# Kernel tuning notes

Hardware: AMD Instinct MI355X
Metric: run time of the kernel (lower is better)

## Reference

```python
import jax, jax.numpy as jnp
import numpy as np

B, S, H, T, E, V, D = 32, 128, 1024, 32, 512, 32000, 256


def setup_inputs() -> dict:
    key = jax.random.key(0)
    ks = jax.random.split(key, 12)
    rn = lambda k, shp, s: jax.random.normal(k, shp, dtype=jnp.float32) * s
    return {
        "fusion_vector": rn(ks[0], (B, S, H), 1.0),
        "hidden_vector": rn(ks[1], (B, H), 1.0),
        "ground_truth_answer_input": rn(ks[2], (B, T, E), 1.0),
        "ground_truth_seq_helper": T,
        "U_w": rn(ks[3], (D, H), 0.02), "U_b": jnp.zeros((D,), jnp.float32),
        "V_w": rn(ks[4], (D, H), 0.02), "V_b": jnp.zeros((D,), jnp.float32),
        "P_w": rn(ks[5], (1, D), 0.02), "P_b": jnp.zeros((1,), jnp.float32),
        "W_ih": rn(ks[6], (3 * H, E + H), 0.02), "b_ih": jnp.zeros((3 * H,), jnp.float32),
        "W_hh": rn(ks[7], (3 * H, H), 0.02), "b_hh": jnp.zeros((3 * H,), jnp.float32),
        "dense_w": rn(ks[8], (V, H), 0.02), "dense_b": jnp.zeros((V,), jnp.float32),
    }


def reference(fusion_vector, hidden_vector, ground_truth_answer_input,
              U_w, U_b, V_w, V_b, P_w, P_b,
              W_ih, b_ih, W_hh, b_hh, dense_w, dense_b,
              ground_truth_seq_helper):
    f = fusion_vector                                  # (B, S, H)
    # V(f) is loop-invariant: precompute tanh(V f) once.
    vf = jnp.tanh(jnp.einsum('bsh,dh->bsd', f, V_w) + V_b)  # (B, S, D)

    def step(h, x):
        # Bilinear attention pooling: q = h (decoder hidden state)
        uh = jnp.tanh(h @ U_w.T + U_b)                 # (B, D)
        scores = jnp.einsum('bsd,d->bs', uh[:, None, :] * vf, P_w[0]) + P_b[0]
        attn = jax.nn.softmax(scores, axis=-1)         # (B, S)
        mix = jnp.einsum('bs,bsh->bh', attn, f)        # (B, H)
        inp = jnp.concatenate([x, mix], axis=1)        # (B, E+H)
        # torch GRUCell: gate order r, z, n
        gx = inp @ W_ih.T + b_ih
        gh = h @ W_hh.T + b_hh
        xr, xz, xn = jnp.split(gx, 3, axis=1)
        hr, hz, hn = jnp.split(gh, 3, axis=1)
        r = jax.nn.sigmoid(xr + hr)
        z = jax.nn.sigmoid(xz + hz)
        n = jnp.tanh(xn + r * hn)
        h_new = (1.0 - z) * n + z * h
        logits = h_new @ dense_w.T + dense_b           # (B, V)
        return h_new, logits

    xs = jnp.swapaxes(ground_truth_answer_input[:, :-1, :], 0, 1)  # (T-1, B, E)
    _, logits = jax.lax.scan(step, hidden_vector, xs)              # (T-1, B, V)
    return jnp.swapaxes(logits, 0, 1)                              # (B, T-1, V)
```

## Files before the change

kernel.cpp:

```cpp
#include <hip/hip_runtime.h>
#include <hip/hip_bf16.h>
#include <math.h>

typedef unsigned short u16;
typedef unsigned long long u64;
typedef __attribute__((ext_vector_type(8))) short short8;
typedef __attribute__((ext_vector_type(4))) float f32x4;
typedef __attribute__((ext_vector_type(2))) _Float16 half2v;

static __device__ __forceinline__ u16 f2b(float x) {
  __hip_bfloat16 h = __float2bfloat16(x);
  return *reinterpret_cast<u16*>(&h);
}
static __device__ __forceinline__ float b2f(u16 u) {
  unsigned int v = ((unsigned int)u) << 16;
  float f;
  __builtin_memcpy(&f, &v, 4);
  return f;
}
static __device__ __forceinline__ u16 f2h(float x) {
  _Float16 h = (_Float16)x;
  u16 u;
  __builtin_memcpy(&u, &h, 2);
  return u;
}
static __device__ __forceinline__ float dot2(unsigned w, unsigned h, float acc) {
  half2v a, b;
  __builtin_memcpy(&a, &w, 4);
  __builtin_memcpy(&b, &h, 4);
#if __has_builtin(__builtin_amdgcn_fdot2)
  return __builtin_amdgcn_fdot2(a, b, acc, false);
#else
  return acc + (float)a[0] * (float)b[0] + (float)a[1] * (float)b[1];
#endif
}

static __device__ __forceinline__ float aldf(const float* p) {
  return __hip_atomic_load(const_cast<float*>(p), __ATOMIC_RELAXED, __HIP_MEMORY_SCOPE_AGENT);
}
static __device__ __forceinline__ void astf(float* p, float v) {
  __hip_atomic_store(p, v, __ATOMIC_RELAXED, __HIP_MEMORY_SCOPE_AGENT);
}
static __device__ __forceinline__ u64 ald8(const u64* p) {
  return __hip_atomic_load(const_cast<u64*>(p), __ATOMIC_RELAXED, __HIP_MEMORY_SCOPE_AGENT);
}
static __device__ __forceinline__ void ast32(unsigned* p, unsigned v) {
  __hip_atomic_store(p, v, __ATOMIC_RELAXED, __HIP_MEMORY_SCOPE_AGENT);
}


__global__ void cvt_flat(const float* __restrict__ s, u16* __restrict__ d, long n) {
  long i = ((long)blockIdx.x * 256 + threadIdx.x) * 4;
  long stride = (long)gridDim.x * 1024;
  for (; i < n; i += stride) {
    float4 v = *(const float4*)(s + i);
    ushort4 o;
    o.x = f2b(v.x); o.y = f2b(v.y); o.z = f2b(v.z); o.w = f2b(v.w);
    *(ushort4*)(d + i) = o;
  }
}

__global__ void cvt_packh(const float* __restrict__ s, unsigned* __restrict__ d, long npairs) {
  long i = (long)blockIdx.x * 256 + threadIdx.x;
  long step = (long)gridDim.x * 256;
  for (; i < npairs; i += step) {
    float2 v = *(const float2*)(s + 2 * i);
    d[i] = (unsigned)f2h(v.x) | ((unsigned)f2h(v.y) << 16);
  }
}

__global__ void cvt_strided(const float* __restrict__ s, u16* __restrict__ d,
                            long total, int lshift, long sstride, long soff) {
  long i = (long)blockIdx.x * 256 + threadIdx.x;
  long step = (long)gridDim.x * 256;
  long mask = (1L << lshift) - 1;
  for (; i < total; i += step) {
    long r = i >> lshift;
    long c = i & mask;
    d[i] = f2b(s[r * sstride + soff + c]);
  }
}

__global__ void cvt_x(const float* __restrict__ gt, u16* __restrict__ d) {
  long idx = (long)blockIdx.x * 256 + threadIdx.x;
  if (idx >= 1024L * 512) return;
  long m = idx >> 9;
  int k = (int)(idx & 511);
  if (m < 992) {
    int tt = (int)(m >> 5), b = (int)(m & 31);
    d[idx] = f2b(gt[((long)b * 32 + tt) * 512 + k]);
  } else {
    d[idx] = 0;
  }
}

template<int EPI>
__global__ __launch_bounds__(256)
void gemm_bt(const u16* __restrict__ A, const u16* __restrict__ B,
             void* __restrict__ C0,
             const float* __restrict__ bias, const float* __restrict__ pw,
             int M, int N, int K) {
  __shared__ u16 As[4096];
  __shared__ u16 Bs[4096];
  const int tid = threadIdx.x;
  const int lane = tid & 63, wid = tid >> 6;

  int gx = gridDim.x, gy = gridDim.y;
  int orig = blockIdx.y * gx + blockIdx.x;
  int G = gx < 8 ? gx : 8;
  int ng = gx / G;
  int full = ng * G * gy;
  int ct, rt;
  if (orig < full) {
    int grp = orig / (G * gy), rem = orig % (G * gy);
    ct = grp * G + rem % G;
    rt = rem / G;
  } else {
    int Gt = gx - ng * G;
    int rem = orig - full;
    ct = ng * G + rem % Gt;
    rt = rem / Gt;
  }
  const long row0 = (long)rt * 128;
  const long col0 = (long)ct * 128;

  const int wm = (wid >> 1) * 64, wn = (wid & 1) * 64;
  const int fr = lane & 15, fq = lane >> 4;
  const int sr = wid * 16 + (lane >> 2);
  const int sc = (lane & 3) * 8;

  const u16* Ag0 = A + (row0 + sr) * (long)K + sc;
  const u16* Ag1 = Ag0 + 64 * (long)K;
  const u16* Bg0 = B + (col0 + sr) * (long)K + sc;
  const u16* Bg1 = Bg0 + 64 * (long)K;

  u16* AsW0 = &As[wid * 512];
  u16* AsW1 = &As[2048 + wid * 512];
  u16* BsW0 = &Bs[wid * 512];
  u16* BsW1 = &Bs[2048 + wid * 512];

  f32x4 acc[4][4];
#pragma unroll
  for (int i = 0; i < 4; ++i)
#pragma unroll
    for (int j = 0; j < 4; ++j) acc[i][j] = {0.f, 0.f, 0.f, 0.f};

  for (int k0 = 0; k0 < K; k0 += 32) {
    __builtin_amdgcn_global_load_lds((const __attribute__((address_space(1))) void*)(Ag0 + k0),
                                     (__attribute__((address_space(3))) void*)AsW0, 16, 0, 0);
    __builtin_amdgcn_global_load_lds((const __attribute__((address_space(1))) void*)(Ag1 + k0),
                                     (__attribute__((address_space(3))) void*)AsW1, 16, 0, 0);
    __builtin_amdgcn_global_load_lds((const __attribute__((address_space(1))) void*)(Bg0 + k0),
                                     (__attribute__((address_space(3))) void*)BsW0, 16, 0, 0);
    __builtin_amdgcn_global_load_lds((const __attribute__((address_space(1))) void*)(Bg1 + k0),
                                     (__attribute__((address_space(3))) void*)BsW1, 16, 0, 0);
    __syncthreads();
    short8 af[4], bfv[4];
#pragma unroll
    for (int i = 0; i < 4; ++i) af[i] = *(const short8*)&As[(wm + i * 16 + fr) * 32 + fq * 8];
#pragma unroll
    for (int i = 0; i < 4; ++i) bfv[i] = *(const short8*)&Bs[(wn + i * 16 + fr) * 32 + fq * 8];
#pragma unroll
    for (int i = 0; i < 4; ++i)
#pragma unroll
      for (int j = 0; j < 4; ++j)
        acc[i][j] = __builtin_amdgcn_mfma_f32_16x16x32_bf16(af[i], bfv[j], acc[i][j], 0, 0, 0);
    __syncthreads();
  }

#pragma unroll
  for (int i = 0; i < 4; ++i)
#pragma unroll
    for (int j = 0; j < 4; ++j)
#pragma unroll
      for (int q = 0; q < 4; ++q) {
        long gr = row0 + wm + i * 16 + fq * 4 + q;
        long gc = col0 + wn + j * 16 + fr;
        float v = acc[i][j][q];
        if constexpr (EPI == 0) {
          ((u16*)C0)[gr * (long)N + gc] = f2b(v);
        } else if constexpr (EPI == 1) {
          ((u16*)C0)[gr * (long)N + gc] = f2b(tanhf(v + bias[gc]) * pw[gc]);
        } else if constexpr (EPI == 2) {
          if (gr < M) ((float*)C0)[gr * (long)N + gc] = v + bias[gc];
        } else {
          if (gr < M) {
            long bb = gr & 31, tt = gr >> 5;
            float o = v + bias[gc];
            __builtin_nontemporal_store(o, &((float*)C0)[(bb * 31 + tt) * (long)N + gc]);
          }
        }
      }
}

__global__ __launch_bounds__(1024)
void persist(const unsigned* __restrict__ WcatH, const float* __restrict__ bcat,
             const u16* __restrict__ wvfb, const u16* __restrict__ FWb,
             const float* __restrict__ GX, const float* __restrict__ pbv,
             const float* __restrict__ h0,
             unsigned* __restrict__ hG32, float* __restrict__ gates,
             u16* __restrict__ Hbuf, unsigned* __restrict__ cnt) {
  const int tid = threadIdx.x;
  const int blk = blockIdx.x;
  const int rg = blk >> 2, bg = blk & 3;
  const int b = blk >> 3, jc = blk & 7;

  __shared__ unsigned wlds[52 * 516];
  __shared__ float hl2[128];
  __shared__ __align__(16) char smem[45056];
  unsigned* hlds = (unsigned*)smem;
  float*    plds = (float*)(smem + 16512 * 4 / 4 + 0);
  plds = (float*)(smem + 16512);
  float* uhl   = (float*)smem;
  float* part  = uhl + 256;
  float* attnv = part + 1024;
  float* gmp   = attnv + 128;

  const float pb0 = pbv[0];
  if (tid < 128) hl2[tid] = h0[b * 1024 + jc * 128 + tid];

  for (int it = tid; it < 52 * 512; it += 1024) {
    int row = it >> 9, idx = it & 511;
    wlds[row * 516 + idx] = WcatH[(long)(rg * 52 + row) * 512 + idx];
  }

  auto xbar = [&](unsigned target) {
    __syncthreads();
    if (tid == 0) {
      __hip_atomic_fetch_add(cnt, 1u, __ATOMIC_RELAXED, __HIP_MEMORY_SCOPE_AGENT);
      while (__hip_atomic_load(cnt, __ATOMIC_RELAXED, __HIP_MEMORY_SCOPE_AGENT) < target) {
        __builtin_amdgcn_s_sleep(2);
      }
    }
    __syncthreads();
  };
  xbar(256u);

  for (int t = 0; t < 31; ++t) {
    {
      long base = (long)(bg * 8) * 512;
      int g = tid * 4;
      u64 v0 = ald8((const u64*)(hG32 + base + g));
      u64 v1 = ald8((const u64*)(hG32 + base + g + 2));
      int bi = g >> 9, idx = g & 511;
      unsigned* dst = hlds + bi * 516 + idx;
      dst[0] = (unsigned)v0; dst[1] = (unsigned)(v0 >> 32);
      dst[2] = (unsigned)v1; dst[3] = (unsigned)(v1 >> 32);
    }
    __syncthreads();
    {
      const int akc = tid >> 6, w = tid & 63;
      const int bl = w & 7, rch = w >> 3;
      uint4 hv[8];
      const uint4* hp = (const uint4*)(hlds + bl * 516 + akc * 32);
#pragma unroll
      for (int j = 0; j < 8; ++j) hv[j] = hp[j];
#pragma unroll
      for (int i = 0; i < 7; ++i) {
        int rl = rch * 7 + i;
        if (rl < 52) {
          const uint4* wp = (const uint4*)(wlds + rl * 516 + akc * 32);
          float acc = 0.f;
#pragma unroll
          for (int j = 0; j < 8; ++j) {
            uint4 w4 = wp[j];
            acc = dot2(w4.x, hv[j].x, acc);
            acc = dot2(w4.y, hv[j].y, acc);
            acc = dot2(w4.z, hv[j].z, acc);
            acc = dot2(w4.w, hv[j].w, acc);
          }
          plds[(rl * 8 + bl) * 17 + akc] = acc;
        }
      }
    }
    __syncthreads();
    if (tid < 416) {
      const float* pp = plds + tid * 17;
      float s = 0.f;
#pragma unroll
      for (int k = 0; k < 16; ++k) s += pp[k];
      int rl = tid >> 3, bl = tid & 7;
      astf(gates + (long)(bg * 8 + bl) * 3328 + rg * 52 + rl, s);
    }
    xbar(256u * (2 * t + 2));

    if (tid < 128) {
      u64 v = ald8((const u64*)(gates + (long)b * 3328 + tid * 2));
      float2 f2v;
      __builtin_memcpy(&f2v, &v, 8);
      uhl[tid * 2] = tanhf(f2v.x + bcat[tid * 2]);
      uhl[tid * 2 + 1] = tanhf(f2v.y + bcat[tid * 2 + 1]);
    }
    __syncthreads();
    {
      const int s = tid & 127, q = tid >> 7;
      const u16* wr = wvfb + ((long)(b * 128 + s)) * 256 + q * 32;
      const float* uq = &uhl[q * 32];
      float p = 0.f;
#pragma unroll
      for (int d = 0; d < 32; d += 8) {
        short8 wv = *(const short8*)(wr + d);
#pragma unroll
        for (int e = 0; e < 8; ++e) p += b2f((u16)wv[e]) * uq[d + e];
      }
      part[tid] = p;
    }
    __syncthreads();
    if (tid < 128) {
      float s8 = pb0;
#pragma unroll
      for (int j = 0; j < 8; ++j) s8 += part[tid + 128 * j];
      attnv[tid] = s8;
    }
    __syncthreads();
    if (tid < 64) {
      float m = fmaxf(attnv[tid], attnv[tid + 64]);
#pragma unroll
      for (int o = 32; o; o >>= 1) m = fmaxf(m, __shfl_xor(m, o));
      float e0 = expf(attnv[tid] - m), e1 = expf(attnv[tid + 64] - m);
      float s2 = e0 + e1;
#pragma unroll
      for (int o = 32; o; o >>= 1) s2 += __shfl_xor(s2, o);
      float inv = 1.f / s2;
      attnv[tid] = e0 * inv;
      attnv[tid + 64] = e1 * inv;
    }
    __syncthreads();
    {
      const int ml = tid & 127, sh = tid >> 7;
      const int col = jc * 128 + ml;
      float g0 = 0.f, g1 = 0.f, g2 = 0.f;
      const u16* fw = FWb + ((long)(b * 128 + sh * 16)) * 3072 + col;
#pragma unroll 4
      for (int s = 0; s < 16; ++s) {
        float a = attnv[sh * 16 + s];
        g0 += a * b2f(fw[0]);
        g1 += a * b2f(fw[1024]);
        g2 += a * b2f(fw[2048]);
        fw += 3072;
      }
      gmp[0 * 1024 + tid] = g0;
      gmp[1 * 1024 + tid] = g1;
      gmp[2 * 1024 + tid] = g2;
    }
    __syncthreads();
    if (tid < 128) {
      const int m = jc * 128 + tid;
      float gm0 = 0.f, gm1 = 0.f, gm2 = 0.f;
#pragma unroll
      for (int j = 0; j < 8; ++j) {
        gm0 += gmp[0 * 1024 + tid + 128 * j];
        gm1 += gmp[1 * 1024 + tid + 128 * j];
        gm2 += gmp[2 * 1024 + tid + 128 * j];
      }
      float gh0 = aldf(gates + (long)b * 3328 + 256 + m) + bcat[256 + m];
      float gh1 = aldf(gates + (long)b * 3328 + 1280 + m) + bcat[1280 + m];
      float gh2 = aldf(gates + (long)b * 3328 + 2304 + m) + bcat[2304 + m];
      const long gxo = ((long)t * 32 + b) * 3072;
      float xr = GX[gxo + m] + gm0;
      float xz = GX[gxo + 1024 + m] + gm1;
      float xn = GX[gxo + 2048 + m] + gm2;
      float r = 1.f / (1.f + expf(-(xr + gh0)));
      float z = 1.f / (1.f + expf(-(xz + gh1)));
      float n = tanhf(xn + r * gh2);
      float h2 = (1.f - z) * n + z * hl2[tid];
      hl2[tid] = h2;
      Hbuf[((long)t * 32 + b) * 1024 + m] = f2b(h2);
      float hp = __shfl_xor(h2, 1);
      if ((tid & 1) == 0) {
        unsigned pk = (unsigned)f2h(h2) | ((unsigned)f2h(hp) << 16);
        ast32(hG32 + (long)b * 512 + jc * 64 + (tid >> 1), pk);
      }
    }
    xbar(256u * (2 * t + 3));
  }
}


extern "C" void kernel_launch(void* const* d_in, const int* in_sizes, int n_in,
                              void* d_out, int out_size, void* d_ws, size_t ws_size,
                              hipStream_t stream) {
  const float* f    = (const float*)d_in[0];
  const float* h0   = (const float*)d_in[1];
  const float* gt   = (const float*)d_in[2];
  const float* U_w  = (const float*)d_in[4];
  const float* U_b  = (const float*)d_in[5];
  const float* V_w  = (const float*)d_in[6];
  const float* V_b  = (const float*)d_in[7];
  const float* P_w  = (const float*)d_in[8];
  const float* P_b  = (const float*)d_in[9];
  const float* W_ih = (const float*)d_in[10];
  const float* b_ih = (const float*)d_in[11];
  const float* W_hh = (const float*)d_in[12];
  const float* b_hh = (const float*)d_in[13];
  const float* dw   = (const float*)d_in[14];
  const float* db   = (const float*)d_in[15];

  char* w = (char*)d_ws;
  auto alloc = [&](size_t bytes) { char* p = w; w += (bytes + 255) & ~255ULL; return p; };

  u16*      fbf   = (u16*)alloc(4096L * 1024 * 2);
  u16*      VwB   = (u16*)alloc(256L * 1024 * 2);
  unsigned* WcatH = (unsigned*)alloc(3328L * 512 * 4);
  u16*      WxB   = (u16*)alloc(3072L * 512 * 2);
  u16*      WmB   = (u16*)alloc(3072L * 1024 * 2);
  u16*      dwB   = (u16*)alloc(32000L * 1024 * 2);
  u16*      Xb    = (u16*)alloc(1024L * 512 * 2);
  u16*      wvfb  = (u16*)alloc(4096L * 256 * 2);
  float*    GX    = (float*)alloc(1024L * 3072 * 4);
  u16*      FWb   = (u16*)alloc(4096L * 3072 * 2);
  unsigned* hG32  = (unsigned*)alloc(32L * 512 * 4);
  float*    gates = (float*)alloc(32L * 3328 * 4);
  u16*      Hbuf  = (u16*)alloc(1024L * 1024 * 2);
  float*    bcat  = (float*)alloc(3328L * 4);
  unsigned* cnt   = (unsigned*)alloc(256);

  auto cvg = [](long n) { long g = (n + 1023) / 1024; return (int)(g > 2048 ? 2048 : g); };

  cvt_flat<<<cvg(4194304), 256, 0, stream>>>(f, fbf, 4194304);
  cvt_flat<<<cvg(262144), 256, 0, stream>>>(V_w, VwB, 262144);
  cvt_packh<<<512, 256, 0, stream>>>(U_w, WcatH, 131072);
  cvt_packh<<<2048, 256, 0, stream>>>(W_hh, WcatH + 131072, 1572864);
  cvt_packh<<<64, 256, 0, stream>>>(h0, hG32, 16384);
  cvt_strided<<<2048, 256, 0, stream>>>(W_ih, WxB, 3072L * 512, 9, 1536, 0);
  cvt_strided<<<2048, 256, 0, stream>>>(W_ih, WmB, 3072L * 1024, 10, 1536, 512);
  cvt_flat<<<cvg(32768000), 256, 0, stream>>>(dw, dwB, 32768000);
  cvt_x<<<2048, 256, 0, stream>>>(gt, Xb);
  hipMemcpyAsync(bcat, U_b, 256 * 4, hipMemcpyDeviceToDevice, stream);
  hipMemcpyAsync(bcat + 256, b_hh, 3072 * 4, hipMemcpyDeviceToDevice, stream);
  hipMemsetAsync(cnt, 0, 4, stream);

  gemm_bt<1><<<dim3(2, 32), 256, 0, stream>>>(fbf, VwB, wvfb, V_b, P_w, 4096, 256, 1024);
  gemm_bt<2><<<dim3(24, 8), 256, 0, stream>>>(Xb, WxB, GX, b_ih, nullptr, 992, 3072, 512);
  gemm_bt<0><<<dim3(24, 32), 256, 0, stream>>>(fbf, WmB, FWb, nullptr, nullptr, 4096, 3072, 1024);

  {
    void* ka[] = {(void*)&WcatH, (void*)&bcat, (void*)&wvfb, (void*)&FWb,
                  (void*)&GX,    (void*)&P_b,  (void*)&h0,   (void*)&hG32,
                  (void*)&gates, (void*)&Hbuf, (void*)&cnt};
    hipLaunchCooperativeKernel((void*)persist, dim3(256), dim3(1024), ka, 0, stream);
  }

  gemm_bt<3><<<dim3(250, 8), 256, 0, stream>>>(Hbuf, dwB, (float*)d_out, db, nullptr,
                                               992, 32000, 1024);
}
```

Measured before the change: 826.4 us.

## Transpose FW gate buffer for vector loads and use hierarchical grid barrier

The FW precompute GEMM now writes its output transposed (column-major over the 4096 rows), so the persistent kernel's attention-mix step reads 16 contiguous bf16 values per gate with two 16-byte loads instead of 16 strided scalar loads. The single global atomic barrier counter is replaced by a two-level barrier: per-group counters for 8 blocks, plus a root counter bumped by the last arriver of each group, which cuts contention on one address. The transposed epilogue store in the GEMM becomes strided and less coalesced, and the barrier adds an extra atomic hop on the critical path.

Result: slower. 1.058 ms (+28.0%).

```diff
diff --git a/kernel.cpp b/kernel.cpp
--- a/kernel.cpp
+++ b/kernel.cpp
@@ -178,7 +178,7 @@
         long gc = col0 + wn + j * 16 + fr;
         float v = acc[i][j][q];
         if constexpr (EPI == 0) {
-          ((u16*)C0)[gr * (long)N + gc] = f2b(v);
+          ((u16*)C0)[gc * 4096L + gr] = f2b(v);
         } else if constexpr (EPI == 1) {
           ((u16*)C0)[gr * (long)N + gc] = f2b(tanhf(v + bias[gc]) * pw[gc]);
         } else if constexpr (EPI == 2) {
@@ -195,7 +195,7 @@
 
 __global__ __launch_bounds__(1024)
 void persist(const unsigned* __restrict__ WcatH, const float* __restrict__ bcat,
-             const u16* __restrict__ wvfb, const u16* __restrict__ FWb,
+             const u16* __restrict__ wvfb, const u16* __restrict__ FWt,
              const float* __restrict__ GX, const float* __restrict__ pbv,
              const float* __restrict__ h0,
              unsigned* __restrict__ hG32, float* __restrict__ gates,
@@ -209,8 +209,7 @@
   __shared__ float hl2[128];
   __shared__ __align__(16) char smem[45056];
   unsigned* hlds = (unsigned*)smem;
-  float*    plds = (float*)(smem + 16512 * 4 / 4 + 0);
-  plds = (float*)(smem + 16512);
+  float*    plds = (float*)(smem + 16512);
   float* uhl   = (float*)smem;
   float* part  = uhl + 256;
   float* attnv = part + 1024;
@@ -224,17 +223,25 @@
     wlds[row * 516 + idx] = WcatH[(long)(rg * 52 + row) * 512 + idx];
   }
 
-  auto xbar = [&](unsigned target) {
+  unsigned phctr = 0;
+  auto xbar = [&]() {
+    ++phctr;
     __syncthreads();
     if (tid == 0) {
-      __hip_atomic_fetch_add(cnt, 1u, __ATOMIC_RELAXED, __HIP_MEMORY_SCOPE_AGENT);
-      while (__hip_atomic_load(cnt, __ATOMIC_RELAXED, __HIP_MEMORY_SCOPE_AGENT) < target) {
+      unsigned* gp = cnt + 16 * (blk >> 3);
+      unsigned* root = cnt + 16 * 32;
+      unsigned v = __hip_atomic_fetch_add(gp, 1u, __ATOMIC_RELAXED,
+                                          __HIP_MEMORY_SCOPE_AGENT) + 1;
+      if (v == 8u * phctr)
+        __hip_atomic_fetch_add(root, 1u, __ATOMIC_RELAXED, __HIP_MEMORY_SCOPE_AGENT);
+      while (__hip_atomic_load(root, __ATOMIC_RELAXED, __HIP_MEMORY_SCOPE_AGENT) <
+             32u * phctr) {
         __builtin_amdgcn_s_sleep(2);
       }
     }
     __syncthreads();
   };
-  xbar(256u);
+  xbar();
 
   for (int t = 0; t < 31; ++t) {
     {
@@ -282,7 +289,7 @@
       int rl = tid >> 3, bl = tid & 7;
       astf(gates + (long)(bg * 8 + bl) * 3328 + rg * 52 + rl, s);
     }
-    xbar(256u * (2 * t + 2));
+    xbar();
 
     if (tid < 128) {
       u64 v = ald8((const u64*)(gates + (long)b * 3328 + tid * 2));
@@ -330,18 +337,19 @@
       const int ml = tid & 127, sh = tid >> 7;
       const int col = jc * 128 + ml;
       float g0 = 0.f, g1 = 0.f, g2 = 0.f;
-      const u16* fw = FWb + ((long)(b * 128 + sh * 16)) * 3072 + col;
-#pragma unroll 4
-      for (int s = 0; s < 16; ++s) {
-        float a = attnv[sh * 16 + s];
-        g0 += a * b2f(fw[0]);
-        g1 += a * b2f(fw[1024]);
-        g2 += a * b2f(fw[2048]);
-        fw += 3072;
-      }
-      gmp[0 * 1024 + tid] = g0;
-      gmp[1 * 1024 + tid] = g1;
-      gmp[2 * 1024 + tid] = g2;
+      const float* at = &attnv[sh * 16];
+#pragma unroll
+      for (int g = 0; g < 3; ++g) {
+        const u16* fw = FWt + ((long)(g * 1024 + col)) * 4096 + b * 128 + sh * 16;
+        short8 v0 = *(const short8*)fw;
+        short8 v1 = *(const short8*)(fw + 8);
+        float acc = 0.f;
+#pragma unroll
+        for (int e = 0; e < 8; ++e) acc += at[e] * b2f((u16)v0[e]);
+#pragma unroll
+        for (int e = 0; e < 8; ++e) acc += at[8 + e] * b2f((u16)v1[e]);
+        gmp[g * 1024 + tid] = acc;
+      }
     }
     __syncthreads();
     if (tid < 128) {
@@ -372,7 +380,7 @@
         ast32(hG32 + (long)b * 512 + jc * 64 + (tid >> 1), pk);
       }
     }
-    xbar(256u * (2 * t + 3));
+    xbar();
   }
 }
 
@@ -408,12 +416,12 @@
   u16*      Xb    = (u16*)alloc(1024L * 512 * 2);
   u16*      wvfb  = (u16*)alloc(4096L * 256 * 2);
   float*    GX    = (float*)alloc(1024L * 3072 * 4);
-  u16*      FWb   = (u16*)alloc(4096L * 3072 * 2);
+  u16*      FWt   = (u16*)alloc(3072L * 4096 * 2);
   unsigned* hG32  = (unsigned*)alloc(32L * 512 * 4);
   float*    gates = (float*)alloc(32L * 3328 * 4);
   u16*      Hbuf  = (u16*)alloc(1024L * 1024 * 2);
   float*    bcat  = (float*)alloc(3328L * 4);
-  unsigned* cnt   = (unsigned*)alloc(256);
+  unsigned* cnt   = (unsigned*)alloc(4096);
 
   auto cvg = [](long n) { long g = (n + 1023) / 1024; return (int)(g > 2048 ? 2048 : g); };
 
@@ -428,14 +436,14 @@
   cvt_x<<<2048, 256, 0, stream>>>(gt, Xb);
   hipMemcpyAsync(bcat, U_b, 256 * 4, hipMemcpyDeviceToDevice, stream);
   hipMemcpyAsync(bcat + 256, b_hh, 3072 * 4, hipMemcpyDeviceToDevice, stream);
-  hipMemsetAsync(cnt, 0, 4, stream);
+  hipMemsetAsync(cnt, 0, 4096, stream);
 
   gemm_bt<1><<<dim3(2, 32), 256, 0, stream>>>(fbf, VwB, wvfb, V_b, P_w, 4096, 256, 1024);
   gemm_bt<2><<<dim3(24, 8), 256, 0, stream>>>(Xb, WxB, GX, b_ih, nullptr, 992, 3072, 512);
-  gemm_bt<0><<<dim3(24, 32), 256, 0, stream>>>(fbf, WmB, FWb, nullptr, nullptr, 4096, 3072, 1024);
+  gemm_bt<0><<<dim3(24, 32), 256, 0, stream>>>(fbf, WmB, FWt, nullptr, nullptr, 4096, 3072, 1024);
 
   {
-    void* ka[] = {(void*)&WcatH, (void*)&bcat, (void*)&wvfb, (void*)&FWb,
+    void* ka[] = {(void*)&WcatH, (void*)&bcat, (void*)&wvfb, (void*)&FWt,
                   (void*)&GX,    (void*)&P_b,  (void*)&h0,   (void*)&hG32,
                   (void*)&gates, (void*)&Hbuf, (void*)&cnt};
     hipLaunchCooperativeKernel((void*)persist, dim3(256), dim3(1024), ka, 0, stream);
```
